# Performance work log

Hardware: AMD Instinct MI355X
Metric: run time of the kernel (lower is better)

## Reference

```python
import jax, jax.numpy as jnp
import numpy as np


def setup_inputs() -> dict:
    key = jax.random.key(0)
    ks = jax.random.split(key, 6)
    B, T, D, H = 2, 2048, 1024, 16
    dk = D // H
    s = 0.02
    return {
        "x": jax.random.normal(ks[0], (B, T, D), dtype=jnp.float32),
        "Wq": jax.random.normal(ks[1], (H, dk, dk), dtype=jnp.float32) * s,
        "Wk": jax.random.normal(ks[2], (H, dk, dk), dtype=jnp.float32) * s,
        "Wv": jax.random.normal(ks[3], (H, dk, dk), dtype=jnp.float32) * s,
        "Wp": jax.random.normal(ks[4], (D, D), dtype=jnp.float32) * s,
        "bp": jnp.zeros((D,), dtype=jnp.float32),
    }


def reference(x, Wq, Wk, Wv, Wp, bp):
    B, T, D = x.shape
    H, dk, _ = Wq.shape
    # split into heads: [B, H, T, dk]
    xh = x.reshape(B, T, H, dk).transpose(0, 2, 1, 3)
    # per-head torch Linear (y = x @ W^T), all heads at once
    q = jnp.einsum('bhtd,hkd->bhtk', xh, Wq)
    k = jnp.einsum('bhtd,hkd->bhtk', xh, Wk)
    v = jnp.einsum('bhtd,hkd->bhtk', xh, Wv)
    scale = 1.0 / jnp.sqrt(jnp.float32(dk))  # original divides by sqrt(C) with C == d_k
    scores = jnp.einsum('bhqd,bhkd->bhqk', q, k) * scale
    causal = jnp.tril(jnp.ones((T, T), dtype=bool))
    scores = jnp.where(causal[None, None], scores, -jnp.inf)
    attn = jax.nn.softmax(scores, axis=-1)
    out = jnp.einsum('bhqk,bhkd->bhqd', attn, v)  # [B,H,T,dk]
    out = out.transpose(0, 2, 1, 3).reshape(B, T, D)  # concat heads
    return out @ Wp.T + bp
```

## Files before the change

kernel.cpp:

```cpp
#include <hip/hip_runtime.h>
#include <math.h>

#define B_ 2
#define T_ 2048
#define D_ 1024
#define H_ 16
#define DK 64
#define BH_ (B_*H_)

typedef __attribute__((ext_vector_type(8))) short short8;
typedef __attribute__((ext_vector_type(4))) short bf16x4;
typedef __attribute__((ext_vector_type(4))) float fragC;

__device__ __forceinline__ unsigned short f2bf(float x) {
    union { float f; unsigned u; } c; c.f = x;
    unsigned r = c.u + 0x7fff + ((c.u >> 16) & 1);
    return (unsigned short)(r >> 16);
}

__device__ __forceinline__ unsigned short f2bf_trunc(float x) {
    union { float f; unsigned u; } c; c.f = x;
    return (unsigned short)(c.u >> 16);
}

__device__ __forceinline__ unsigned pack2bf(float a, float b) {
    return (unsigned)f2bf(a) | ((unsigned)f2bf(b) << 16);
}

__device__ __forceinline__ int swz(int row, int unit) {
    return row*64 + (((unit ^ (row & 7)) << 3));
}

__device__ __forceinline__ void gload_lds16(const void* g, void* l) {
    __builtin_amdgcn_global_load_lds(
        (const __attribute__((address_space(1))) unsigned int*)g,
        (__attribute__((address_space(3))) unsigned int*)l, 16, 0, 0);
}

__global__ __launch_bounds__(256) void cvt_kernel(
    const float* __restrict__ x, const float* __restrict__ Wp,
    const float* __restrict__ Wq, const float* __restrict__ Wk,
    const float* __restrict__ Wv,
    unsigned short* __restrict__ xb, unsigned short* __restrict__ Wb,
    unsigned short* __restrict__ wqkvb)
{
    const int gid = blockIdx.x * 256 + threadIdx.x;
    const float* src; unsigned short* dst;
    if (gid < 524288)      { src = x  + (size_t)gid * 8;            dst = xb + (size_t)gid * 8; }
    else if (gid < 655360) { int e = gid - 524288;
                             src = Wp + (size_t)e * 8;              dst = Wb + (size_t)e * 8; }
    else                   { int e = gid - 655360;
                             int mat = e >> 13, rem = e & 8191;
                             int h = rem >> 9, od = rem & 511;
                             const float* ws = (mat == 0) ? Wq : (mat == 1) ? Wk : Wv;
                             src = ws + ((size_t)(h << 9) + od) * 8;
                             dst = wqkvb + ((size_t)h*1536 + mat*512 + od) * 8; }
    float4 a = *(const float4*)src;
    float4 b = *(const float4*)(src + 4);
    *(uint4*)dst = make_uint4(pack2bf(a.x, a.y), pack2bf(a.z, a.w),
                              pack2bf(b.x, b.y), pack2bf(b.z, b.w));
}

__global__ __launch_bounds__(256) void qkv_kernel(
    const unsigned short* __restrict__ xb,
    const unsigned short* __restrict__ wqkvb,
    unsigned short* __restrict__ q, unsigned short* __restrict__ k,
    unsigned short* __restrict__ vt)
{
    __shared__ unsigned short Wl[3*64*64];

    const int bh = blockIdx.x;
    const int b  = bh >> 4, h = bh & 15;
    const int t0 = blockIdx.y * 128;
    const int tid = threadIdx.x;
    const int wave = tid >> 6, lane = tid & 63;
    const int n = lane & 15, quad = lane >> 4;

    {
        const unsigned short* wsrc = wqkvb + (size_t)h * 12288;
        #pragma unroll
        for (int j = 0; j < 6; ++j) {
            const int off = (wave*6 + j) * 512 + lane*8;
            gload_lds16(wsrc + off, &Wl[off]);
        }
    }

    const int tw = t0 + wave*32;
    short8 xf[2][2];
    #pragma unroll
    for (int rt = 0; rt < 2; ++rt) {
        const unsigned short* xr = &xb[((size_t)b*T_ + tw + rt*16 + n)*D_ + h*DK];
        xf[rt][0] = *(const short8*)&xr[quad*8];
        xf[rt][1] = *(const short8*)&xr[32 + quad*8];
    }
    __syncthreads();

    #pragma unroll
    for (int mat = 0; mat < 3; ++mat) {
        const int wbase = mat * 4096;
        #pragma unroll
        for (int ct = 0; ct < 4; ++ct) {
            short8 wf0 = *(const short8*)&Wl[wbase + (ct*16 + n)*64 + quad*8];
            short8 wf1 = *(const short8*)&Wl[wbase + (ct*16 + n)*64 + 32 + quad*8];
            #pragma unroll
            for (int rt = 0; rt < 2; ++rt) {
                fragC z = {0.f,0.f,0.f,0.f};
                if (mat < 2) {
                    z = __builtin_amdgcn_mfma_f32_16x16x32_bf16(wf0, xf[rt][0], z, 0,0,0);
                    z = __builtin_amdgcn_mfma_f32_16x16x32_bf16(wf1, xf[rt][1], z, 0,0,0);
                    unsigned short* dstg = (mat == 0) ? q : k;
                    unsigned short* dp = &dstg[((size_t)bh*T_ + tw + rt*16 + n)*DK
                                               + ct*16 + quad*4];
                    *(uint2*)dp = make_uint2(pack2bf(z[0], z[1]), pack2bf(z[2], z[3]));
                } else {
                    z = __builtin_amdgcn_mfma_f32_16x16x32_bf16(xf[rt][0], wf0, z, 0,0,0);
                    z = __builtin_amdgcn_mfma_f32_16x16x32_bf16(xf[rt][1], wf1, z, 0,0,0);
                    unsigned short* dp = &vt[((size_t)bh*DK + ct*16 + n)*T_
                                             + tw + rt*16 + quad*4];
                    *(uint2*)dp = make_uint2(pack2bf(z[0], z[1]), pack2bf(z[2], z[3]));
                }
            }
        }
    }
}

__global__ __launch_bounds__(256, 2) void attn_kernel(
    const unsigned short* __restrict__ q, const unsigned short* __restrict__ k,
    const unsigned short* __restrict__ vt, unsigned short* __restrict__ aout)
{
    __shared__ unsigned short Ks[64*64];
    __shared__ unsigned short Vs[64*64];
    __shared__ unsigned short Ps[4][16][68];

    const int id = blockIdx.x;
    int qt, bh;
    if (id < 256) { bh = id >> 3;         qt = 15 - (id & 7); }
    else          { bh = (id - 256) >> 3; qt = (id - 256) & 7; }

    const int b   = bh >> 4, h = bh & 15;
    const int tid = threadIdx.x;
    const int wave = tid >> 6, lane = tid & 63;
    const int n = lane & 15, quad = lane >> 4;

    const size_t qkbase = (size_t)bh * T_ * DK;
    const int q0 = qt*128 + wave*32;

    short8 qf[2][2];
    #pragma unroll
    for (int rt = 0; rt < 2; ++rt) {
        qf[rt][0] = *(const short8*)&q[qkbase + (size_t)(q0 + rt*16 + n)*DK + quad*8];
        qf[rt][1] = *(const short8*)&q[qkbase + (size_t)(q0 + rt*16 + n)*DK + 32 + quad*8];
    }

    fragC o[2][4];
    #pragma unroll
    for (int rt = 0; rt < 2; ++rt)
        #pragma unroll
        for (int dt = 0; dt < 4; ++dt) o[rt][dt] = (fragC){0.f,0.f,0.f,0.f};
    fragC l4[2] = {(fragC){0.f,0.f,0.f,0.f}, (fragC){0.f,0.f,0.f,0.f}};

    short8 ones;
    #pragma unroll
    for (int j = 0; j < 8; ++j) ones[j] = (short)0x3F80;

    const int srow = tid >> 2;
    const int u0   = (tid & 3) * 2;
    const unsigned short* kg = &k[qkbase + (size_t)srow*DK + u0*8];
    const unsigned short* vg = &vt[((size_t)bh*DK + srow)*T_ + u0*8];
    const int kl0 = swz(srow, u0), kl1 = swz(srow, u0+1);

    const int nt = 2*qt + 2;
    short8 pk0 = *(const short8*)&kg[0], pk1 = *(const short8*)&kg[8];
    short8 pv0 = *(const short8*)&vg[0], pv1 = *(const short8*)&vg[8];

    const float sc = 0.125f * 1.44269504088896340736f;

    for (int kt = 0; kt < nt; ++kt) {
        __syncthreads();
        *(short8*)&Ks[kl0] = pk0; *(short8*)&Ks[kl1] = pk1;
        *(short8*)&Vs[kl0] = pv0; *(short8*)&Vs[kl1] = pv1;
        __syncthreads();
        if (kt + 1 < nt) {
            pk0 = *(const short8*)&kg[(size_t)(kt+1)*64*DK];
            pk1 = *(const short8*)&kg[(size_t)(kt+1)*64*DK + 8];
            pv0 = *(const short8*)&vg[(kt+1)*64];
            pv1 = *(const short8*)&vg[(kt+1)*64 + 8];
        }
        const int k0 = kt * 64;
        if (k0 > q0 + 31) continue;

        #pragma unroll
        for (int rt = 0; rt < 2; ++rt) {
            const bool diag = (k0 + 63 > q0 + rt*16);
            #pragma unroll
            for (int ct = 0; ct < 4; ++ct) {
                const int row = ct*16 + n;
                short8 kf0 = *(const short8*)&Ks[swz(row, quad)];
                short8 kf1 = *(const short8*)&Ks[swz(row, 4 + quad)];
                fragC c = {0.f,0.f,0.f,0.f};
                c = __builtin_amdgcn_mfma_f32_16x16x32_bf16(kf0, qf[rt][0], c, 0,0,0);
                c = __builtin_amdgcn_mfma_f32_16x16x32_bf16(kf1, qf[rt][1], c, 0,0,0);
                float p[4];
                #pragma unroll
                for (int r = 0; r < 4; ++r) p[r] = exp2f(c[r] * sc);
                if (diag) {
                    const int lim = (q0 + rt*16 + n) - (k0 + ct*16 + quad*4);
                    #pragma unroll
                    for (int r = 0; r < 4; ++r) if (r > lim) p[r] = 0.f;
                }
                union { uint2 u; unsigned short s[4]; } w;
                w.s[0] = f2bf_trunc(p[0]); w.s[1] = f2bf_trunc(p[1]);
                w.s[2] = f2bf_trunc(p[2]); w.s[3] = f2bf_trunc(p[3]);
                *(uint2*)&Ps[wave][n][ct*16 + quad*4] = w.u;
            }
            bf16x4 a0 = *(const bf16x4*)&Ps[wave][n][quad*8];
            bf16x4 a1 = *(const bf16x4*)&Ps[wave][n][quad*8 + 4];
            bf16x4 a2 = *(const bf16x4*)&Ps[wave][n][32 + quad*8];
            bf16x4 a3 = *(const bf16x4*)&Ps[wave][n][32 + quad*8 + 4];
            short8 pf0 = __builtin_shufflevector(a0, a1, 0,1,2,3,4,5,6,7);
            short8 pf1 = __builtin_shufflevector(a2, a3, 0,1,2,3,4,5,6,7);
            l4[rt] = __builtin_amdgcn_mfma_f32_16x16x32_bf16(ones, pf0, l4[rt], 0,0,0);
            l4[rt] = __builtin_amdgcn_mfma_f32_16x16x32_bf16(ones, pf1, l4[rt], 0,0,0);
            #pragma unroll
            for (int dt = 0; dt < 4; ++dt) {
                const int row = dt*16 + n;
                short8 vf0 = *(const short8*)&Vs[swz(row, quad)];
                short8 vf1 = *(const short8*)&Vs[swz(row, 4 + quad)];
                o[rt][dt] = __builtin_amdgcn_mfma_f32_16x16x32_bf16(vf0, pf0, o[rt][dt], 0,0,0);
                o[rt][dt] = __builtin_amdgcn_mfma_f32_16x16x32_bf16(vf1, pf1, o[rt][dt], 0,0,0);
            }
        }
    }

    #pragma unroll
    for (int rt = 0; rt < 2; ++rt) {
        const float inv = 1.0f / l4[rt][0];
        unsigned short* dp = &aout[((size_t)b*T_ + q0 + rt*16 + n)*D_ + h*DK + quad*4];
        #pragma unroll
        for (int dt = 0; dt < 4; ++dt) {
            *(uint2*)(dp + dt*16) =
                make_uint2(pack2bf(o[rt][dt][0]*inv, o[rt][dt][1]*inv),
                           pack2bf(o[rt][dt][2]*inv, o[rt][dt][3]*inv));
        }
    }
}

__global__ __launch_bounds__(256) void proj_kernel(
    const unsigned short* __restrict__ A, const unsigned short* __restrict__ Wb,
    const float* __restrict__ bp, float* __restrict__ out)
{
    __shared__ unsigned short As[128*64];
    __shared__ unsigned short Bs[128*64];

    const int m0 = blockIdx.x * 128, n0 = blockIdx.y * 128;
    const int tid = threadIdx.x;
    const int wave = tid >> 6, lane = tid & 63;
    const int wm = wave & 1, wn = wave >> 1;
    const int n = lane & 15, quad = lane >> 4;

    const int srow = wave*32 + (lane >> 3);
    const int scol = (lane & 7) * 8;
    const unsigned short* ag = &A [(size_t)(m0 + srow)*1024 + scol];
    const unsigned short* bg = &Wb[(size_t)(n0 + srow)*1024 + scol];
    unsigned short* al = &As[(size_t)srow*64 + scol];
    unsigned short* bl = &Bs[(size_t)srow*64 + scol];

    fragC acc[4][4];
    #pragma unroll
    for (int i = 0; i < 4; ++i)
        #pragma unroll
        for (int j = 0; j < 4; ++j) acc[i][j] = (fragC){0.f,0.f,0.f,0.f};

    for (int kt = 0; kt < 16; ++kt) {
        __syncthreads();
        #pragma unroll
        for (int i = 0; i < 4; ++i) {
            gload_lds16(ag + (size_t)i*8*1024 + kt*64, al + i*8*64);
            gload_lds16(bg + (size_t)i*8*1024 + kt*64, bl + i*8*64);
        }
        __syncthreads();

        #pragma unroll
        for (int kk = 0; kk < 2; ++kk) {
            short8 af[4], bf[4];
            #pragma unroll
            for (int i = 0; i < 4; ++i)
                af[i] = *(const short8*)&As[(wm*64 + i*16 + n)*64 + kk*32 + quad*8];
            #pragma unroll
            for (int j = 0; j < 4; ++j)
                bf[j] = *(const short8*)&Bs[(wn*64 + j*16 + n)*64 + kk*32 + quad*8];
            #pragma unroll
            for (int i = 0; i < 4; ++i)
                #pragma unroll
                for (int j = 0; j < 4; ++j)
                    acc[i][j] = __builtin_amdgcn_mfma_f32_16x16x32_bf16(af[i], bf[j], acc[i][j], 0,0,0);
        }
    }

    #pragma unroll
    for (int i = 0; i < 4; ++i) {
        #pragma unroll
        for (int r = 0; r < 4; ++r) {
            const int m = m0 + wm*64 + i*16 + quad*4 + r;
            #pragma unroll
            for (int j = 0; j < 4; ++j) {
                const int col = n0 + wn*64 + j*16 + n;
                out[(size_t)m*1024 + col] = acc[i][j][r] + bp[col];
            }
        }
    }
}

extern "C" void kernel_launch(void* const* d_in, const int* in_sizes, int n_in,
                              void* d_out, int out_size, void* d_ws, size_t ws_size,
                              hipStream_t stream)
{
    const float* x  = (const float*)d_in[0];
    const float* Wq = (const float*)d_in[1];
    const float* Wk = (const float*)d_in[2];
    const float* Wv = (const float*)d_in[3];
    const float* Wp = (const float*)d_in[4];
    const float* bp = (const float*)d_in[5];
    float* out = (float*)d_out;

    const size_t per = (size_t)BH_ * T_ * DK;
    unsigned short* qws   = (unsigned short*)d_ws;
    unsigned short* kws   = qws + per;
    unsigned short* vtws  = kws + per;
    unsigned short* aws   = vtws + per;
    unsigned short* wbws  = aws + per;
    unsigned short* xbws  = wbws + 1024*1024;
    unsigned short* wqkvb = xbws + per;

    cvt_kernel<<<dim3(2656), 256, 0, stream>>>(x, Wp, Wq, Wk, Wv, xbws, wbws, wqkvb);
    qkv_kernel<<<dim3(BH_, T_/128), 256, 0, stream>>>(xbws, wqkvb, qws, kws, vtws);
    attn_kernel<<<dim3(512), 256, 0, stream>>>(qws, kws, vtws, aws);
    proj_kernel<<<dim3(32, 8), 256, 0, stream>>>(aws, wbws, bp, out);
}
```

Measured before the change: 159.8 us.

## Fuse x bf16 conversion into QKV, retile attention to 64-row query blocks, fragment-major Q/K

```diff
diff --git a/kernel.cpp b/kernel.cpp
--- a/kernel.cpp
+++ b/kernel.cpp
@@ -27,6 +27,13 @@
     return (unsigned)f2bf(a) | ((unsigned)f2bf(b) << 16);
 }
 
+__device__ __forceinline__ short8 packbf8(float4 a, float4 b) {
+    union { short8 v; unsigned u[4]; } r;
+    r.u[0] = pack2bf(a.x, a.y); r.u[1] = pack2bf(a.z, a.w);
+    r.u[2] = pack2bf(b.x, b.y); r.u[3] = pack2bf(b.z, b.w);
+    return r.v;
+}
+
 __device__ __forceinline__ int swz(int row, int unit) {
     return row*64 + (((unit ^ (row & 7)) << 3));
 }
@@ -38,23 +45,20 @@
 }
 
 __global__ __launch_bounds__(256) void cvt_kernel(
-    const float* __restrict__ x, const float* __restrict__ Wp,
+    const float* __restrict__ Wp,
     const float* __restrict__ Wq, const float* __restrict__ Wk,
     const float* __restrict__ Wv,
-    unsigned short* __restrict__ xb, unsigned short* __restrict__ Wb,
-    unsigned short* __restrict__ wqkvb)
+    unsigned short* __restrict__ Wb, unsigned short* __restrict__ wqkvb)
 {
     const int gid = blockIdx.x * 256 + threadIdx.x;
     const float* src; unsigned short* dst;
-    if (gid < 524288)      { src = x  + (size_t)gid * 8;            dst = xb + (size_t)gid * 8; }
-    else if (gid < 655360) { int e = gid - 524288;
-                             src = Wp + (size_t)e * 8;              dst = Wb + (size_t)e * 8; }
-    else                   { int e = gid - 655360;
-                             int mat = e >> 13, rem = e & 8191;
-                             int h = rem >> 9, od = rem & 511;
-                             const float* ws = (mat == 0) ? Wq : (mat == 1) ? Wk : Wv;
-                             src = ws + ((size_t)(h << 9) + od) * 8;
-                             dst = wqkvb + ((size_t)h*1536 + mat*512 + od) * 8; }
+    if (gid < 131072) { src = Wp + (size_t)gid * 8; dst = Wb + (size_t)gid * 8; }
+    else              { int e = gid - 131072;
+                        int mat = e >> 13, rem = e & 8191;
+                        int h = rem >> 9, od = rem & 511;
+                        const float* ws = (mat == 0) ? Wq : (mat == 1) ? Wk : Wv;
+                        src = ws + ((size_t)(h << 9) + od) * 8;
+                        dst = wqkvb + ((size_t)h*1536 + mat*512 + od) * 8; }
     float4 a = *(const float4*)src;
     float4 b = *(const float4*)(src + 4);
     *(uint4*)dst = make_uint4(pack2bf(a.x, a.y), pack2bf(a.z, a.w),
@@ -62,7 +66,7 @@
 }
 
 __global__ __launch_bounds__(256) void qkv_kernel(
-    const unsigned short* __restrict__ xb,
+    const float* __restrict__ x,
     const unsigned short* __restrict__ wqkvb,
     unsigned short* __restrict__ q, unsigned short* __restrict__ k,
     unsigned short* __restrict__ vt)
@@ -89,12 +93,17 @@
     short8 xf[2][2];
     #pragma unroll
     for (int rt = 0; rt < 2; ++rt) {
-        const unsigned short* xr = &xb[((size_t)b*T_ + tw + rt*16 + n)*D_ + h*DK];
-        xf[rt][0] = *(const short8*)&xr[quad*8];
-        xf[rt][1] = *(const short8*)&xr[32 + quad*8];
+        const float* xr = &x[((size_t)b*T_ + tw + rt*16 + n)*D_ + h*DK];
+        float4 a0 = *(const float4*)&xr[quad*8];
+        float4 a1 = *(const float4*)&xr[quad*8 + 4];
+        xf[rt][0] = packbf8(a0, a1);
+        float4 b0 = *(const float4*)&xr[32 + quad*8];
+        float4 b1 = *(const float4*)&xr[32 + quad*8 + 4];
+        xf[rt][1] = packbf8(b0, b1);
     }
     __syncthreads();
 
+    const int tb0 = blockIdx.y*8 + wave*2;
     #pragma unroll
     for (int mat = 0; mat < 3; ++mat) {
         const int wbase = mat * 4096;
@@ -109,8 +118,8 @@
                     z = __builtin_amdgcn_mfma_f32_16x16x32_bf16(wf0, xf[rt][0], z, 0,0,0);
                     z = __builtin_amdgcn_mfma_f32_16x16x32_bf16(wf1, xf[rt][1], z, 0,0,0);
                     unsigned short* dstg = (mat == 0) ? q : k;
-                    unsigned short* dp = &dstg[((size_t)bh*T_ + tw + rt*16 + n)*DK
-                                               + ct*16 + quad*4];
+                    unsigned short* dp = &dstg[((size_t)bh*128 + tb0 + rt)*1024
+                                               + (ct*2 + (quad>>1))*128 + n*8 + (quad&1)*4];
                     *(uint2*)dp = make_uint2(pack2bf(z[0], z[1]), pack2bf(z[2], z[3]));
                 } else {
                     z = __builtin_amdgcn_mfma_f32_16x16x32_bf16(xf[rt][0], wf0, z, 0,0,0);
@@ -124,7 +133,7 @@
     }
 }
 
-__global__ __launch_bounds__(256, 2) void attn_kernel(
+__global__ __launch_bounds__(256, 4) void attn_kernel(
     const unsigned short* __restrict__ q, const unsigned short* __restrict__ k,
     const unsigned short* __restrict__ vt, unsigned short* __restrict__ aout)
 {
@@ -134,30 +143,24 @@
 
     const int id = blockIdx.x;
     int qt, bh;
-    if (id < 256) { bh = id >> 3;         qt = 15 - (id & 7); }
-    else          { bh = (id - 256) >> 3; qt = (id - 256) & 7; }
+    if (id < 512) { bh = id >> 4;         qt = 31 - (id & 15); }
+    else          { bh = (id - 512) >> 4; qt = (id - 512) & 15; }
 
     const int b   = bh >> 4, h = bh & 15;
     const int tid = threadIdx.x;
     const int wave = tid >> 6, lane = tid & 63;
     const int n = lane & 15, quad = lane >> 4;
 
-    const size_t qkbase = (size_t)bh * T_ * DK;
-    const int q0 = qt*128 + wave*32;
-
-    short8 qf[2][2];
-    #pragma unroll
-    for (int rt = 0; rt < 2; ++rt) {
-        qf[rt][0] = *(const short8*)&q[qkbase + (size_t)(q0 + rt*16 + n)*DK + quad*8];
-        qf[rt][1] = *(const short8*)&q[qkbase + (size_t)(q0 + rt*16 + n)*DK + 32 + quad*8];
-    }
-
-    fragC o[2][4];
-    #pragma unroll
-    for (int rt = 0; rt < 2; ++rt)
-        #pragma unroll
-        for (int dt = 0; dt < 4; ++dt) o[rt][dt] = (fragC){0.f,0.f,0.f,0.f};
-    fragC l4[2] = {(fragC){0.f,0.f,0.f,0.f}, (fragC){0.f,0.f,0.f,0.f}};
+    const int q0 = qt*64 + wave*16;
+
+    const unsigned short* qb = &q[((size_t)bh*128 + qt*4 + wave)*1024 + n*8];
+    short8 qf0 = *(const short8*)&qb[quad*128];
+    short8 qf1 = *(const short8*)&qb[(4 + quad)*128];
+
+    fragC o[4];
+    #pragma unroll
+    for (int dt = 0; dt < 4; ++dt) o[dt] = (fragC){0.f,0.f,0.f,0.f};
+    fragC l4 = {0.f,0.f,0.f,0.f};
 
     short8 ones;
     #pragma unroll
@@ -165,12 +168,13 @@
 
     const int srow = tid >> 2;
     const int u0   = (tid & 3) * 2;
-    const unsigned short* kg = &k[qkbase + (size_t)srow*DK + u0*8];
+    const unsigned short* kg = &k[(size_t)bh*131072
+                                  + (srow >> 4)*1024 + u0*128 + (srow & 15)*8];
     const unsigned short* vg = &vt[((size_t)bh*DK + srow)*T_ + u0*8];
     const int kl0 = swz(srow, u0), kl1 = swz(srow, u0+1);
 
-    const int nt = 2*qt + 2;
-    short8 pk0 = *(const short8*)&kg[0], pk1 = *(const short8*)&kg[8];
+    const int nt = qt + 1;
+    short8 pk0 = *(const short8*)&kg[0], pk1 = *(const short8*)&kg[128];
     short8 pv0 = *(const short8*)&vg[0], pv1 = *(const short8*)&vg[8];
 
     const float sc = 0.125f * 1.44269504088896340736f;
@@ -181,67 +185,59 @@
         *(short8*)&Vs[kl0] = pv0; *(short8*)&Vs[kl1] = pv1;
         __syncthreads();
         if (kt + 1 < nt) {
-            pk0 = *(const short8*)&kg[(size_t)(kt+1)*64*DK];
-            pk1 = *(const short8*)&kg[(size_t)(kt+1)*64*DK + 8];
+            pk0 = *(const short8*)&kg[(size_t)(kt+1)*4096];
+            pk1 = *(const short8*)&kg[(size_t)(kt+1)*4096 + 128];
             pv0 = *(const short8*)&vg[(kt+1)*64];
             pv1 = *(const short8*)&vg[(kt+1)*64 + 8];
         }
-        const int k0 = kt * 64;
-        if (k0 > q0 + 31) continue;
-
-        #pragma unroll
-        for (int rt = 0; rt < 2; ++rt) {
-            const bool diag = (k0 + 63 > q0 + rt*16);
-            #pragma unroll
-            for (int ct = 0; ct < 4; ++ct) {
-                const int row = ct*16 + n;
-                short8 kf0 = *(const short8*)&Ks[swz(row, quad)];
-                short8 kf1 = *(const short8*)&Ks[swz(row, 4 + quad)];
-                fragC c = {0.f,0.f,0.f,0.f};
-                c = __builtin_amdgcn_mfma_f32_16x16x32_bf16(kf0, qf[rt][0], c, 0,0,0);
-                c = __builtin_amdgcn_mfma_f32_16x16x32_bf16(kf1, qf[rt][1], c, 0,0,0);
-                float p[4];
+        const bool diag = (kt == qt);
+
+        #pragma unroll
+        for (int ct = 0; ct < 4; ++ct) {
+            const int row = ct*16 + n;
+            short8 kf0 = *(const short8*)&Ks[swz(row, quad)];
+            short8 kf1 = *(const short8*)&Ks[swz(row, 4 + quad)];
+            fragC c = {0.f,0.f,0.f,0.f};
+            c = __builtin_amdgcn_mfma_f32_16x16x32_bf16(kf0, qf0, c, 0,0,0);
+            c = __builtin_amdgcn_mfma_f32_16x16x32_bf16(kf1, qf1, c, 0,0,0);
+            float p[4];
+            #pragma unroll
+            for (int r = 0; r < 4; ++r) p[r] = exp2f(c[r] * sc);
+            if (diag) {
+                const int lim = (wave*16 + n) - (ct*16 + quad*4);
                 #pragma unroll
-                for (int r = 0; r < 4; ++r) p[r] = exp2f(c[r] * sc);
-                if (diag) {
-                    const int lim = (q0 + rt*16 + n) - (k0 + ct*16 + quad*4);
-                    #pragma unroll
-                    for (int r = 0; r < 4; ++r) if (r > lim) p[r] = 0.f;
-                }
-                union { uint2 u; unsigned short s[4]; } w;
-                w.s[0] = f2bf_trunc(p[0]); w.s[1] = f2bf_trunc(p[1]);
-                w.s[2] = f2bf_trunc(p[2]); w.s[3] = f2bf_trunc(p[3]);
-                *(uint2*)&Ps[wave][n][ct*16 + quad*4] = w.u;
+                for (int r = 0; r < 4; ++r) if (r > lim) p[r] = 0.f;
             }
-            bf16x4 a0 = *(const bf16x4*)&Ps[wave][n][quad*8];
-            bf16x4 a1 = *(const bf16x4*)&Ps[wave][n][quad*8 + 4];
-            bf16x4 a2 = *(const bf16x4*)&Ps[wave][n][32 + quad*8];
-            bf16x4 a3 = *(const bf16x4*)&Ps[wave][n][32 + quad*8 + 4];
-            short8 pf0 = __builtin_shufflevector(a0, a1, 0,1,2,3,4,5,6,7);
-            short8 pf1 = __builtin_shufflevector(a2, a3, 0,1,2,3,4,5,6,7);
-            l4[rt] = __builtin_amdgcn_mfma_f32_16x16x32_bf16(ones, pf0, l4[rt], 0,0,0);
-            l4[rt] = __builtin_amdgcn_mfma_f32_16x16x32_bf16(ones, pf1, l4[rt], 0,0,0);
-            #pragma unroll
-            for (int dt = 0; dt < 4; ++dt) {
-                const int row = dt*16 + n;
-                short8 vf0 = *(const short8*)&Vs[swz(row, quad)];
-                short8 vf1 = *(const short8*)&Vs[swz(row, 4 + quad)];
-                o[rt][dt] = __builtin_amdgcn_mfma_f32_16x16x32_bf16(vf0, pf0, o[rt][dt], 0,0,0);
-                o[rt][dt] = __builtin_amdgcn_mfma_f32_16x16x32_bf16(vf1, pf1, o[rt][dt], 0,0,0);
-            }
-        }
-    }
-
-    #pragma unroll
-    for (int rt = 0; rt < 2; ++rt) {
-        const float inv = 1.0f / l4[rt][0];
-        unsigned short* dp = &aout[((size_t)b*T_ + q0 + rt*16 + n)*D_ + h*DK + quad*4];
+            union { uint2 u; unsigned short s[4]; } w;
+            w.s[0] = f2bf_trunc(p[0]); w.s[1] = f2bf_trunc(p[1]);
+            w.s[2] = f2bf_trunc(p[2]); w.s[3] = f2bf_trunc(p[3]);
+            *(uint2*)&Ps[wave][n][ct*16 + quad*4] = w.u;
+        }
+        bf16x4 a0 = *(const bf16x4*)&Ps[wave][n][quad*8];
+        bf16x4 a1 = *(const bf16x4*)&Ps[wave][n][quad*8 + 4];
+        bf16x4 a2 = *(const bf16x4*)&Ps[wave][n][32 + quad*8];
+        bf16x4 a3 = *(const bf16x4*)&Ps[wave][n][32 + quad*8 + 4];
+        short8 pf0 = __builtin_shufflevector(a0, a1, 0,1,2,3,4,5,6,7);
+        short8 pf1 = __builtin_shufflevector(a2, a3, 0,1,2,3,4,5,6,7);
+        l4 = __builtin_amdgcn_mfma_f32_16x16x32_bf16(ones, pf0, l4, 0,0,0);
+        l4 = __builtin_amdgcn_mfma_f32_16x16x32_bf16(ones, pf1, l4, 0,0,0);
         #pragma unroll
         for (int dt = 0; dt < 4; ++dt) {
-            *(uint2*)(dp + dt*16) =
-                make_uint2(pack2bf(o[rt][dt][0]*inv, o[rt][dt][1]*inv),
-                           pack2bf(o[rt][dt][2]*inv, o[rt][dt][3]*inv));
-        }
+            const int row = dt*16 + n;
+            short8 vf0 = *(const short8*)&Vs[swz(row, quad)];
+            short8 vf1 = *(const short8*)&Vs[swz(row, 4 + quad)];
+            o[dt] = __builtin_amdgcn_mfma_f32_16x16x32_bf16(vf0, pf0, o[dt], 0,0,0);
+            o[dt] = __builtin_amdgcn_mfma_f32_16x16x32_bf16(vf1, pf1, o[dt], 0,0,0);
+        }
+    }
+
+    const float inv = 1.0f / l4[0];
+    unsigned short* dp = &aout[((size_t)b*T_ + q0 + n)*D_ + h*DK + quad*4];
+    #pragma unroll
+    for (int dt = 0; dt < 4; ++dt) {
+        *(uint2*)(dp + dt*16) =
+            make_uint2(pack2bf(o[dt][0]*inv, o[dt][1]*inv),
+                       pack2bf(o[dt][2]*inv, o[dt][3]*inv));
     }
 }
 
@@ -329,11 +325,10 @@
     unsigned short* vtws  = kws + per;
     unsigned short* aws   = vtws + per;
     unsigned short* wbws  = aws + per;
-    unsigned short* xbws  = wbws + 1024*1024;
-    unsigned short* wqkvb = xbws + per;
-
-    cvt_kernel<<<dim3(2656), 256, 0, stream>>>(x, Wp, Wq, Wk, Wv, xbws, wbws, wqkvb);
-    qkv_kernel<<<dim3(BH_, T_/128), 256, 0, stream>>>(xbws, wqkvb, qws, kws, vtws);
-    attn_kernel<<<dim3(512), 256, 0, stream>>>(qws, kws, vtws, aws);
+    unsigned short* wqkvb = wbws + 1024*1024;
+
+    cvt_kernel<<<dim3(608), 256, 0, stream>>>(Wp, Wq, Wk, Wv, wbws, wqkvb);
+    qkv_kernel<<<dim3(BH_, T_/128), 256, 0, stream>>>(x, wqkvb, qws, kws, vtws);
+    attn_kernel<<<dim3(1024), 256, 0, stream>>>(qws, kws, vtws, aws);
     proj_kernel<<<dim3(32, 8), 256, 0, stream>>>(aws, wbws, bp, out);
 }
```

Measured after the change: 153.6 us. -3.9%, faster.
